# Kernel optimization log

Hardware: AMD Instinct MI355X
Metric: run time of the kernel (lower is better)

The kernel has to match this reference:

```python
import jax, jax.numpy as jnp
import numpy as np

N = 262144          # total nodes in batched graph
B = 2048            # number of graphs
IN_DIM = 512        # in_dim == hidden_dim (required by GRUCell usage)
HID = 512
OUT_DIM = 128
TIMESTEPS = 2


def setup_inputs() -> dict:
    key = jax.random.key(0)
    ks = jax.random.split(key, 12)
    s = 0.02
    x = jax.random.normal(ks[0], (N, IN_DIM), dtype=jnp.float32)
    # sorted random segment ids: ragged graph sizes, node -> graph id
    segment_ids = jnp.sort(jax.random.randint(ks[1], (N,), 0, B, dtype=jnp.int32))
    return {
        "x": x,
        "segment_ids": segment_ids,
        "w_att_l": jax.random.normal(ks[2], (IN_DIM,), dtype=jnp.float32) * s,
        "w_att_r": jax.random.normal(ks[3], (IN_DIM,), dtype=jnp.float32) * s,
        "W_node": jax.random.normal(ks[4], (IN_DIM, HID), dtype=jnp.float32) * s,
        "W_ih": jax.random.normal(ks[5], (3 * HID, HID), dtype=jnp.float32) * s,
        "W_hh": jax.random.normal(ks[6], (3 * HID, HID), dtype=jnp.float32) * s,
        "b_ih": jax.random.normal(ks[7], (3 * HID,), dtype=jnp.float32) * s,
        "b_hh": jax.random.normal(ks[8], (3 * HID,), dtype=jnp.float32) * s,
        "W_lin": jax.random.normal(ks[9], (HID, OUT_DIM), dtype=jnp.float32) * s,
        "b_lin": jax.random.normal(ks[10], (OUT_DIM,), dtype=jnp.float32) * s,
    }


def _segment_softmax(alpha, seg, num_segments):
    # numerically stable per-graph softmax over nodes
    m = jax.ops.segment_max(alpha, seg, num_segments=num_segments)
    e = jnp.exp(alpha - m[seg])
    denom = jax.ops.segment_sum(e, seg, num_segments=num_segments)
    return e / denom[seg]


def _gru_cell(inp, h, W_ih, W_hh, b_ih, b_hh):
    gi = inp @ W_ih.T + b_ih          # [B, 3H]
    gh = h @ W_hh.T + b_hh            # [B, 3H]
    gi_r, gi_z, gi_n = jnp.split(gi, 3, axis=-1)
    gh_r, gh_z, gh_n = jnp.split(gh, 3, axis=-1)
    r = jax.nn.sigmoid(gi_r + gh_r)
    z = jax.nn.sigmoid(gi_z + gh_z)
    n = jnp.tanh(gi_n + r * gh_n)
    return (1.0 - z) * n + z * h


def reference(x, segment_ids, w_att_l, w_att_r, W_node, W_ih, W_hh, b_ih, b_hh, W_lin, b_lin):
    seg = segment_ids
    # SumPooling: per-graph sum of node features -> initial GRU hidden state
    out = jax.ops.segment_sum(x, seg, num_segments=B)      # [B, IN_DIM]
    # src_feats (x) are constant across timesteps -> precompute projections
    left_att = x @ w_att_l                                  # [N]
    h_neighbors = x @ W_node                                # [N, HID]
    for _ in range(TIMESTEPS):
        right_att = out @ w_att_r                           # [B]
        alpha = jax.nn.leaky_relu(left_att + right_att[seg], negative_slope=0.01)
        scores = _segment_softmax(alpha, seg, B)            # [N]
        msg = h_neighbors * scores[:, None]                 # [N, HID]
        gat_out = jax.ops.segment_sum(msg, seg, num_segments=B)  # [B, HID]
        h = jax.nn.elu(gat_out)
        # dropout is identity in eval mode
        out = jax.nn.silu(_gru_cell(h, out, W_ih, W_hh, b_ih, b_hh))
    return out @ W_lin + b_lin                              # [B, OUT_DIM]
```

## Files before the change

### kernel.cpp

```cpp
#include <hip/hip_runtime.h>
#include <hip/hip_bf16.h>
#include <cstdint>
#include <cstddef>

#define N_NODES 262144
#define NGRAPH  2048
#define DIM     512
#define HID3    1536
#define OUTD    128

typedef __attribute__((ext_vector_type(8))) short  short8;
typedef __attribute__((ext_vector_type(4))) float  floatx4;
typedef __attribute__((ext_vector_type(2))) float  floatx2;

__device__ inline unsigned short f2bf(float f) {
    union { float f; uint32_t u; } v; v.f = f;
    uint32_t u = v.u;
    return (unsigned short)((u + 0x7fffu + ((u >> 16) & 1u)) >> 16);
}
__device__ inline float bf2f(unsigned short h) {
    union { uint32_t u; float f; } v; v.u = ((uint32_t)h) << 16; return v.f;
}

__device__ __forceinline__ void gload_lds16(const void* g, void* l) {
    __builtin_amdgcn_global_load_lds((const __attribute__((address_space(1))) void*)g,
                                     (__attribute__((address_space(3))) void*)l, 16, 0, 0);
}

__global__ __launch_bounds__(256) void k_prep(const float* __restrict__ Wih,
        const float* __restrict__ Whh, const float* __restrict__ Wnode,
        const int* __restrict__ seg, unsigned short* __restrict__ Wihb,
        unsigned short* __restrict__ Whhb, unsigned short* __restrict__ WnT,
        int* __restrict__ starts) {
    __shared__ float tile[32][33];
    int id = blockIdx.x, t = threadIdx.x;
    if (id < 3072) {
        int i = id * 256 + t; Wihb[i] = f2bf(Wih[i]);
    } else if (id < 6144) {
        int i = (id - 3072) * 256 + t; Whhb[i] = f2bf(Whh[i]);
    } else if (id < 6400) {
        int idx = id - 6144;
        int bx = idx >> 4, by = idx & 15;
        int tx = t & 31, ty = t >> 5;
        for (int r = 0; r < 32; r += 8)
            tile[ty + r][tx] = Wnode[(size_t)(bx * 32 + ty + r) * DIM + by * 32 + tx];
        __syncthreads();
        for (int r = 0; r < 32; r += 8)
            WnT[(size_t)(by * 32 + ty + r) * DIM + bx * 32 + tx] = f2bf(tile[tx][ty + r]);
    } else {
        int b = (id - 6400) * 256 + t;
        if (b <= NGRAPH) {
            int lo = 0, hi = N_NODES;
            while (lo < hi) { int mid = (lo + hi) >> 1; if (seg[mid] < b) lo = mid + 1; else hi = mid; }
            starts[b] = lo;
        }
    }
}

template<bool WRITE_XQ>
__global__ __launch_bounds__(256) void k_init(const float* __restrict__ x,
        const int* __restrict__ starts, const float* __restrict__ watl,
        float* __restrict__ left_att, float* __restrict__ hcur,
        unsigned short* __restrict__ hcur_bf, unsigned char* __restrict__ xq) {
    __shared__ float wl[DIM];
    __shared__ float red[4 * DIM];
    int b = blockIdx.x, t = threadIdx.x;
    wl[t] = watl[t]; wl[t + 256] = watl[t + 256];
    __syncthreads();
    int s = starts[b], e = starts[b + 1];
    int w = t >> 6, lane = t & 63;
    int f0 = lane * 4;
    float acc[8] = {0.f,0.f,0.f,0.f,0.f,0.f,0.f,0.f};

    auto proc = [&](int i, const float4& v0, const float4& v1) {
        acc[0] += v0.x; acc[1] += v0.y; acc[2] += v0.z; acc[3] += v0.w;
        acc[4] += v1.x; acc[5] += v1.y; acc[6] += v1.z; acc[7] += v1.w;
        float dot = v0.x*wl[f0] + v0.y*wl[f0+1] + v0.z*wl[f0+2] + v0.w*wl[f0+3]
                  + v1.x*wl[256+f0] + v1.y*wl[256+f0+1] + v1.z*wl[256+f0+2] + v1.w*wl[256+f0+3];
        #pragma unroll
        for (int off = 32; off > 0; off >>= 1) dot += __shfl_xor(dot, off);
        if (lane == 0) left_att[i] = dot;
        if constexpr (WRITE_XQ) {
            unsigned int q0 = (unsigned int)__builtin_amdgcn_cvt_pk_fp8_f32(v0.x, v0.y, 0, false);
            q0 = (unsigned int)__builtin_amdgcn_cvt_pk_fp8_f32(v0.z, v0.w, (int)q0, true);
            unsigned int q1 = (unsigned int)__builtin_amdgcn_cvt_pk_fp8_f32(v1.x, v1.y, 0, false);
            q1 = (unsigned int)__builtin_amdgcn_cvt_pk_fp8_f32(v1.z, v1.w, (int)q1, true);
            *reinterpret_cast<unsigned int*>(xq + (size_t)i * DIM + f0) = q0;
            *reinterpret_cast<unsigned int*>(xq + (size_t)i * DIM + 256 + f0) = q1;
        }
    };

    int i = s + w;
    for (; i + 4 < e; i += 8) {
        float4 a0 = *reinterpret_cast<const float4*>(x + (size_t)i * DIM + f0);
        float4 a1 = *reinterpret_cast<const float4*>(x + (size_t)i * DIM + 256 + f0);
        float4 b0 = *reinterpret_cast<const float4*>(x + (size_t)(i + 4) * DIM + f0);
        float4 b1 = *reinterpret_cast<const float4*>(x + (size_t)(i + 4) * DIM + 256 + f0);
        proc(i, a0, a1);
        proc(i + 4, b0, b1);
    }
    if (i < e) {
        float4 a0 = *reinterpret_cast<const float4*>(x + (size_t)i * DIM + f0);
        float4 a1 = *reinterpret_cast<const float4*>(x + (size_t)i * DIM + 256 + f0);
        proc(i, a0, a1);
    }

    #pragma unroll
    for (int j = 0; j < 4; j++) {
        red[w * DIM + f0 + j]       = acc[j];
        red[w * DIM + 256 + f0 + j] = acc[4 + j];
    }
    __syncthreads();
    float s0 = red[t]       + red[DIM + t]       + red[2*DIM + t]       + red[3*DIM + t];
    float s1 = red[256 + t] + red[DIM + 256 + t] + red[2*DIM + 256 + t] + red[3*DIM + 256 + t];
    hcur[(size_t)b * DIM + t] = s0;
    hcur[(size_t)b * DIM + 256 + t] = s1;
    hcur_bf[(size_t)b * DIM + t] = f2bf(s0);
    hcur_bf[(size_t)b * DIM + 256 + t] = f2bf(s1);
}

template<bool XQ>
__global__ __launch_bounds__(256) void k_att(const float* __restrict__ x,
        const unsigned char* __restrict__ xq, const float* __restrict__ left,
        const int* __restrict__ starts, const float* __restrict__ hcur,
        const float* __restrict__ watr, unsigned short* __restrict__ swbf) {
    __shared__ float red[4 * DIM];
    __shared__ float rscal[8];
    int b = blockIdx.x, t = threadIdx.x;
    int w = t >> 6, lane = t & 63;

    float p = hcur[(size_t)b * DIM + t] * watr[t] + hcur[(size_t)b * DIM + 256 + t] * watr[256 + t];
    red[t] = p; __syncthreads();
    for (int off = 128; off > 0; off >>= 1) { if (t < off) red[t] += red[t + off]; __syncthreads(); }
    float ra = red[0];
    __syncthreads();

    int s = starts[b], e = starts[b + 1];
    float m = -1e30f;
    for (int i = s + t; i < e; i += 256) {
        float a = left[i] + ra; a = a >= 0.f ? a : 0.01f * a;
        m = fmaxf(m, a);
    }
    red[t] = m; __syncthreads();
    for (int off = 128; off > 0; off >>= 1) { if (t < off) red[t] = fmaxf(red[t], red[t + off]); __syncthreads(); }
    m = red[0];
    __syncthreads();

    float acc[8] = {0.f,0.f,0.f,0.f,0.f,0.f,0.f,0.f};
    float esum = 0.f;
    if constexpr (XQ) {
        int f0 = lane * 8;
        auto qacc = [&](uint2 q, float ev) {
            floatx2 p0 = __builtin_amdgcn_cvt_pk_f32_fp8((int)q.x, false);
            floatx2 p1 = __builtin_amdgcn_cvt_pk_f32_fp8((int)q.x, true);
            floatx2 p2 = __builtin_amdgcn_cvt_pk_f32_fp8((int)q.y, false);
            floatx2 p3 = __builtin_amdgcn_cvt_pk_f32_fp8((int)q.y, true);
            acc[0] += ev * p0[0]; acc[1] += ev * p0[1];
            acc[2] += ev * p1[0]; acc[3] += ev * p1[1];
            acc[4] += ev * p2[0]; acc[5] += ev * p2[1];
            acc[6] += ev * p3[0]; acc[7] += ev * p3[1];
        };
        int i = s + w;
        for (; i + 4 < e; i += 8) {
            uint2 q0 = *reinterpret_cast<const uint2*>(xq + (size_t)i * DIM + f0);
            uint2 q1 = *reinterpret_cast<const uint2*>(xq + (size_t)(i + 4) * DIM + f0);
            float l0 = left[i], l1 = left[i + 4];
            float a0 = l0 + ra; a0 = a0 >= 0.f ? a0 : 0.01f * a0;
            float a1 = l1 + ra; a1 = a1 >= 0.f ? a1 : 0.01f * a1;
            float e0 = __expf(a0 - m), e1 = __expf(a1 - m);
            esum += e0 + e1;
            qacc(q0, e0);
            qacc(q1, e1);
        }
        if (i < e) {
            uint2 q0 = *reinterpret_cast<const uint2*>(xq + (size_t)i * DIM + f0);
            float a0 = left[i] + ra; a0 = a0 >= 0.f ? a0 : 0.01f * a0;
            float e0 = __expf(a0 - m);
            esum += e0;
            qacc(q0, e0);
        }
        #pragma unroll
        for (int j = 0; j < 8; j++) red[w * DIM + f0 + j] = acc[j];
    } else {
        int f0 = lane * 4;
        for (int i = s + w; i < e; i += 4) {
            float a0 = left[i] + ra; a0 = a0 >= 0.f ? a0 : 0.01f * a0;
            float e0 = __expf(a0 - m);
            esum += e0;
            float4 v0 = *reinterpret_cast<const float4*>(x + (size_t)i * DIM + f0);
            float4 v1 = *reinterpret_cast<const float4*>(x + (size_t)i * DIM + 256 + f0);
            acc[0] += e0 * v0.x; acc[1] += e0 * v0.y; acc[2] += e0 * v0.z; acc[3] += e0 * v0.w;
            acc[4] += e0 * v1.x; acc[5] += e0 * v1.y; acc[6] += e0 * v1.z; acc[7] += e0 * v1.w;
        }
        #pragma unroll
        for (int j = 0; j < 4; j++) {
            red[w * DIM + f0 + j]       = acc[j];
            red[w * DIM + 256 + f0 + j] = acc[4 + j];
        }
    }
    #pragma unroll
    for (int off = 32; off > 0; off >>= 1) esum += __shfl_xor(esum, off);
    if (lane == 0) rscal[w] = esum;
    __syncthreads();
    float tot = rscal[0] + rscal[1] + rscal[2] + rscal[3];
    float inv = tot > 0.f ? 1.0f / tot : 0.0f;
    float s0 = (red[t]       + red[DIM + t]       + red[2*DIM + t]       + red[3*DIM + t])       * inv;
    float s1 = (red[256 + t] + red[DIM + 256 + t] + red[2*DIM + 256 + t] + red[3*DIM + 256 + t]) * inv;
    swbf[(size_t)b * DIM + t] = f2bf(s0);
    swbf[(size_t)b * DIM + 256 + t] = f2bf(s1);
}

template<bool ELU_BF>
__global__ __launch_bounds__(256, 2) void k_gemm(const unsigned short* __restrict__ A0,
        const unsigned short* __restrict__ A1, const unsigned short* __restrict__ Wt0,
        const unsigned short* __restrict__ Wt1, float* __restrict__ Cf0,
        float* __restrict__ Cf1, unsigned short* __restrict__ Cbf, int Ncols) {
    __shared__ __align__(16) unsigned short lA[2][128 * 64];
    __shared__ __align__(16) unsigned short lW[2][128 * 64];
    const unsigned short* A  = (blockIdx.z == 0) ? A0  : A1;
    const unsigned short* Wt = (blockIdx.z == 0) ? Wt0 : Wt1;
    float* Cf = (blockIdx.z == 0) ? Cf0 : Cf1;

    int t = threadIdx.x;
    int w = t >> 6, lane = t & 63;
    int wr = w >> 1, wc = w & 1;
    int mbase = blockIdx.x * 128;
    int nbase = blockIdx.y * 128;
    int fr = lane & 15, hi = lane >> 4;
    int swz_r = (fr & 7) << 4;

    int rbase = t >> 3;
    int cole = ((((t & 7) * 16) ^ ((rbase & 7) << 4)) >> 1);
    int ldsoff = t * 16;

    floatx4 acc[4][4];
    #pragma unroll
    for (int m = 0; m < 4; m++)
        #pragma unroll
        for (int n = 0; n < 4; n++) {
            acc[m][n][0] = 0.f; acc[m][n][1] = 0.f; acc[m][n][2] = 0.f; acc[m][n][3] = 0.f;
        }

    const unsigned short* gA = A  + (size_t)(mbase + rbase) * DIM + cole;
    const unsigned short* gW = Wt + (size_t)(nbase + rbase) * DIM + cole;

    auto stage = [&](int kk, int buf) {
        #pragma unroll
        for (int c = 0; c < 4; ++c) {
            gload_lds16(gA + (size_t)(c * 32) * DIM + kk, (char*)&lA[buf][0] + c * 4096 + ldsoff);
            gload_lds16(gW + (size_t)(c * 32) * DIM + kk, (char*)&lW[buf][0] + c * 4096 + ldsoff);
        }
    };

    stage(0, 0);
    __syncthreads();
    int cur = 0;
    for (int it = 0; it < 8; ++it) {
        if (it < 7) stage((it + 1) * 64, cur ^ 1);
        #pragma unroll
        for (int ks = 0; ks < 2; ++ks) {
            short8 af[4], bf[4];
            int bc = (ks * 64 + hi * 16) ^ swz_r;
            #pragma unroll
            for (int m = 0; m < 4; ++m) {
                int row = wr * 64 + m * 16 + fr;
                af[m] = *reinterpret_cast<const short8*>(&lA[cur][(row * 128 + bc) >> 1]);
            }
            #pragma unroll
            for (int n = 0; n < 4; ++n) {
                int row = wc * 64 + n * 16 + fr;
                bf[n] = *reinterpret_cast<const short8*>(&lW[cur][(row * 128 + bc) >> 1]);
            }
            #pragma unroll
            for (int m = 0; m < 4; ++m)
                #pragma unroll
                for (int n = 0; n < 4; ++n)
                    acc[m][n] = __builtin_amdgcn_mfma_f32_16x16x32_bf16(af[m], bf[n], acc[m][n], 0, 0, 0);
        }
        if (it < 7) __syncthreads();
        cur ^= 1;
    }

    int rq = hi * 4;
    #pragma unroll
    for (int m = 0; m < 4; m++) {
        #pragma unroll
        for (int n = 0; n < 4; n++) {
            int col = nbase + wc * 64 + n * 16 + fr;
            #pragma unroll
            for (int r = 0; r < 4; r++) {
                int row = mbase + wr * 64 + m * 16 + rq + r;
                float v = acc[m][n][r];
                if constexpr (ELU_BF) {
                    v = v > 0.f ? v : (__expf(v) - 1.0f);
                    Cbf[(size_t)row * Ncols + col] = f2bf(v);
                } else {
                    Cf[(size_t)row * Ncols + col] = v;
                }
            }
        }
    }
}

__global__ __launch_bounds__(256) void k_gate(const float* __restrict__ gi,
        const float* __restrict__ gh, const float* __restrict__ bih,
        const float* __restrict__ bhh, float* __restrict__ hcur,
        unsigned short* __restrict__ hcur_bf) {
    int idx = blockIdx.x * 256 + threadIdx.x;
    int b = idx >> 9, j = idx & 511;
    size_t gb = (size_t)b * HID3;
    float gir = gi[gb + j]        + bih[j];
    float giz = gi[gb + 512 + j]  + bih[512 + j];
    float gin = gi[gb + 1024 + j] + bih[1024 + j];
    float ghr = gh[gb + j]        + bhh[j];
    float ghz = gh[gb + 512 + j]  + bhh[512 + j];
    float ghn = gh[gb + 1024 + j] + bhh[1024 + j];
    float r = 1.0f / (1.0f + __expf(-(gir + ghr)));
    float z = 1.0f / (1.0f + __expf(-(giz + ghz)));
    float n = tanhf(gin + r * ghn);
    float h = hcur[(size_t)b * DIM + j];
    float nh = (1.0f - z) * n + z * h;
    float out = nh / (1.0f + __expf(-nh));
    hcur[(size_t)b * DIM + j] = out;
    hcur_bf[(size_t)b * DIM + j] = f2bf(out);
}

__global__ __launch_bounds__(128) void k_fin(const float* __restrict__ hcur,
        const float* __restrict__ Wlin, const float* __restrict__ blin,
        float* __restrict__ out) {
    __shared__ float rows[16 * DIM];
    int t = threadIdx.x;
    int b0 = blockIdx.x * 16;
    for (int i = t; i < 16 * DIM / 4; i += 128)
        reinterpret_cast<float4*>(rows)[i] = reinterpret_cast<const float4*>(hcur + (size_t)b0 * DIM)[i];
    __syncthreads();
    float acc[16];
    #pragma unroll
    for (int r = 0; r < 16; r++) acc[r] = 0.f;
    #pragma unroll 4
    for (int k = 0; k < DIM; k++) {
        float wv = Wlin[k * OUTD + t];
        #pragma unroll
        for (int r = 0; r < 16; r++) acc[r] += rows[r * DIM + k] * wv;
    }
    float bl = blin[t];
    #pragma unroll
    for (int r = 0; r < 16; r++) out[(size_t)(b0 + r) * OUTD + t] = acc[r] + bl;
}

extern "C" void kernel_launch(void* const* d_in, const int* in_sizes, int n_in,
                              void* d_out, int out_size, void* d_ws, size_t ws_size,
                              hipStream_t stream) {
    const float* x     = (const float*)d_in[0];
    const int*   seg   = (const int*)d_in[1];
    const float* watl  = (const float*)d_in[2];
    const float* watr  = (const float*)d_in[3];
    const float* Wnode = (const float*)d_in[4];
    const float* Wih   = (const float*)d_in[5];
    const float* Whh   = (const float*)d_in[6];
    const float* bih   = (const float*)d_in[7];
    const float* bhh   = (const float*)d_in[8];
    const float* Wlin  = (const float*)d_in[9];
    const float* blin  = (const float*)d_in[10];
    float* out = (float*)d_out;

    char* ws = (char*)d_ws;
    size_t off = 0;
    auto alloc = [&](size_t bytes) -> void* {
        void* p = ws + off;
        off += bytes;
        off = (off + 255) & ~(size_t)255;
        return p;
    };
    float*          left    = (float*)          alloc((size_t)N_NODES * sizeof(float));
    float*          hcur    = (float*)          alloc((size_t)NGRAPH * DIM * sizeof(float));
    unsigned short* hcurbf  = (unsigned short*) alloc((size_t)NGRAPH * DIM * 2);
    unsigned short* hgbf    = (unsigned short*) alloc((size_t)NGRAPH * DIM * 2);
    unsigned short* swbf    = (unsigned short*) alloc((size_t)NGRAPH * DIM * 2);
    float*          gi      = (float*)          alloc((size_t)NGRAPH * HID3 * sizeof(float));
    float*          gh      = (float*)          alloc((size_t)NGRAPH * HID3 * sizeof(float));
    unsigned short* WnT     = (unsigned short*) alloc((size_t)DIM * DIM * 2);
    unsigned short* Wihb    = (unsigned short*) alloc((size_t)HID3 * DIM * 2);
    unsigned short* Whhb    = (unsigned short*) alloc((size_t)HID3 * DIM * 2);
    unsigned char*  xq      = (unsigned char*)(ws + off);
    bool use_xq = (off + (size_t)N_NODES * DIM) <= ws_size;

    k_prep<<<6409, 256, 0, stream>>>(Wih, Whh, Wnode, seg, Wihb, Whhb, WnT,
                                     (int*)alloc(0));

    int* starts = (int*)alloc((NGRAPH + 1) * sizeof(int));
    xq = (unsigned char*)(ws + off);
    use_xq = (off + (size_t)N_NODES * DIM) <= ws_size;

    if (use_xq)
        k_init<true ><<<NGRAPH, 256, 0, stream>>>(x, starts, watl, left, hcur, hcurbf, xq);
    else
        k_init<false><<<NGRAPH, 256, 0, stream>>>(x, starts, watl, left, hcur, hcurbf, nullptr);

    for (int ts = 0; ts < 2; ts++) {
        if (use_xq)
            k_att<true ><<<NGRAPH, 256, 0, stream>>>(x, xq, left, starts, hcur, watr, swbf);
        else
            k_att<false><<<NGRAPH, 256, 0, stream>>>(x, xq, left, starts, hcur, watr, swbf);
        k_gemm<true ><<<dim3(NGRAPH / 128, DIM / 128, 1), 256, 0, stream>>>(
            swbf, nullptr, WnT, nullptr, nullptr, nullptr, hgbf, DIM);
        k_gemm<false><<<dim3(NGRAPH / 128, HID3 / 128, 2), 256, 0, stream>>>(
            hgbf, hcurbf, Wihb, Whhb, gi, gh, nullptr, HID3);
        k_gate<<<(NGRAPH * DIM) / 256, 256, 0, stream>>>(gi, gh, bih, bhh, hcur, hcurbf);
    }
    k_fin<<<NGRAPH / 16, 128, 0, stream>>>(hcur, Wlin, blin, out);
}
```

Before: 349.5 us.

## Merge Wnode and Whh GEMMs into one launch, vectorize gate, shuffle reductions

The Wnode projection GEMM and the hidden-state Whh GEMM now share one launch through blockIdx.z, since they are independent, and the Wih GEMM runs afterwards. This gives the node GEMM more concurrent blocks and removes one kernel launch's worth of serialization. The GRU gate kernel now processes four elements per thread with vector loads. The attention kernel's block reductions use wave shuffles instead of shared-memory tree loops, and k_init loads x with nontemporal loads. In exchange, the merged launch has idle z=0 blocks that exit early, and the GEMM takes a runtime branch on whether to write the bf16 output.

```diff
diff --git a/kernel.cpp b/kernel.cpp
--- a/kernel.cpp
+++ b/kernel.cpp
@@ -72,19 +72,19 @@
     int f0 = lane * 4;
     float acc[8] = {0.f,0.f,0.f,0.f,0.f,0.f,0.f,0.f};
 
-    auto proc = [&](int i, const float4& v0, const float4& v1) {
-        acc[0] += v0.x; acc[1] += v0.y; acc[2] += v0.z; acc[3] += v0.w;
-        acc[4] += v1.x; acc[5] += v1.y; acc[6] += v1.z; acc[7] += v1.w;
-        float dot = v0.x*wl[f0] + v0.y*wl[f0+1] + v0.z*wl[f0+2] + v0.w*wl[f0+3]
-                  + v1.x*wl[256+f0] + v1.y*wl[256+f0+1] + v1.z*wl[256+f0+2] + v1.w*wl[256+f0+3];
+    auto proc = [&](int i, floatx4 v0, floatx4 v1) {
+        acc[0] += v0[0]; acc[1] += v0[1]; acc[2] += v0[2]; acc[3] += v0[3];
+        acc[4] += v1[0]; acc[5] += v1[1]; acc[6] += v1[2]; acc[7] += v1[3];
+        float dot = v0[0]*wl[f0] + v0[1]*wl[f0+1] + v0[2]*wl[f0+2] + v0[3]*wl[f0+3]
+                  + v1[0]*wl[256+f0] + v1[1]*wl[256+f0+1] + v1[2]*wl[256+f0+2] + v1[3]*wl[256+f0+3];
         #pragma unroll
         for (int off = 32; off > 0; off >>= 1) dot += __shfl_xor(dot, off);
         if (lane == 0) left_att[i] = dot;
         if constexpr (WRITE_XQ) {
-            unsigned int q0 = (unsigned int)__builtin_amdgcn_cvt_pk_fp8_f32(v0.x, v0.y, 0, false);
-            q0 = (unsigned int)__builtin_amdgcn_cvt_pk_fp8_f32(v0.z, v0.w, (int)q0, true);
-            unsigned int q1 = (unsigned int)__builtin_amdgcn_cvt_pk_fp8_f32(v1.x, v1.y, 0, false);
-            q1 = (unsigned int)__builtin_amdgcn_cvt_pk_fp8_f32(v1.z, v1.w, (int)q1, true);
+            unsigned int q0 = (unsigned int)__builtin_amdgcn_cvt_pk_fp8_f32(v0[0], v0[1], 0, false);
+            q0 = (unsigned int)__builtin_amdgcn_cvt_pk_fp8_f32(v0[2], v0[3], (int)q0, true);
+            unsigned int q1 = (unsigned int)__builtin_amdgcn_cvt_pk_fp8_f32(v1[0], v1[1], 0, false);
+            q1 = (unsigned int)__builtin_amdgcn_cvt_pk_fp8_f32(v1[2], v1[3], (int)q1, true);
             *reinterpret_cast<unsigned int*>(xq + (size_t)i * DIM + f0) = q0;
             *reinterpret_cast<unsigned int*>(xq + (size_t)i * DIM + 256 + f0) = q1;
         }
@@ -92,16 +92,16 @@
 
     int i = s + w;
     for (; i + 4 < e; i += 8) {
-        float4 a0 = *reinterpret_cast<const float4*>(x + (size_t)i * DIM + f0);
-        float4 a1 = *reinterpret_cast<const float4*>(x + (size_t)i * DIM + 256 + f0);
-        float4 b0 = *reinterpret_cast<const float4*>(x + (size_t)(i + 4) * DIM + f0);
-        float4 b1 = *reinterpret_cast<const float4*>(x + (size_t)(i + 4) * DIM + 256 + f0);
+        floatx4 a0 = __builtin_nontemporal_load(reinterpret_cast<const floatx4*>(x + (size_t)i * DIM + f0));
+        floatx4 a1 = __builtin_nontemporal_load(reinterpret_cast<const floatx4*>(x + (size_t)i * DIM + 256 + f0));
+        floatx4 b0 = __builtin_nontemporal_load(reinterpret_cast<const floatx4*>(x + (size_t)(i + 4) * DIM + f0));
+        floatx4 b1 = __builtin_nontemporal_load(reinterpret_cast<const floatx4*>(x + (size_t)(i + 4) * DIM + 256 + f0));
         proc(i, a0, a1);
         proc(i + 4, b0, b1);
     }
     if (i < e) {
-        float4 a0 = *reinterpret_cast<const float4*>(x + (size_t)i * DIM + f0);
-        float4 a1 = *reinterpret_cast<const float4*>(x + (size_t)i * DIM + 256 + f0);
+        floatx4 a0 = __builtin_nontemporal_load(reinterpret_cast<const floatx4*>(x + (size_t)i * DIM + f0));
+        floatx4 a1 = __builtin_nontemporal_load(reinterpret_cast<const floatx4*>(x + (size_t)i * DIM + 256 + f0));
         proc(i, a0, a1);
     }
 
@@ -125,26 +125,30 @@
         const int* __restrict__ starts, const float* __restrict__ hcur,
         const float* __restrict__ watr, unsigned short* __restrict__ swbf) {
     __shared__ float red[4 * DIM];
-    __shared__ float rscal[8];
+    __shared__ float rsh[4];
+    __shared__ float rsm[4];
+    __shared__ float rscal[4];
     int b = blockIdx.x, t = threadIdx.x;
     int w = t >> 6, lane = t & 63;
 
     float p = hcur[(size_t)b * DIM + t] * watr[t] + hcur[(size_t)b * DIM + 256 + t] * watr[256 + t];
-    red[t] = p; __syncthreads();
-    for (int off = 128; off > 0; off >>= 1) { if (t < off) red[t] += red[t + off]; __syncthreads(); }
-    float ra = red[0];
-    __syncthreads();
-
+    #pragma unroll
+    for (int off = 32; off > 0; off >>= 1) p += __shfl_xor(p, off);
+    if (lane == 0) rsh[w] = p;
     int s = starts[b], e = starts[b + 1];
+    __syncthreads();
+    float ra = rsh[0] + rsh[1] + rsh[2] + rsh[3];
+
     float m = -1e30f;
     for (int i = s + t; i < e; i += 256) {
         float a = left[i] + ra; a = a >= 0.f ? a : 0.01f * a;
         m = fmaxf(m, a);
     }
-    red[t] = m; __syncthreads();
-    for (int off = 128; off > 0; off >>= 1) { if (t < off) red[t] = fmaxf(red[t], red[t + off]); __syncthreads(); }
-    m = red[0];
-    __syncthreads();
+    #pragma unroll
+    for (int off = 32; off > 0; off >>= 1) m = fmaxf(m, __shfl_xor(m, off));
+    if (lane == 0) rsm[w] = m;
+    __syncthreads();
+    m = fmaxf(fmaxf(rsm[0], rsm[1]), fmaxf(rsm[2], rsm[3]));
 
     float acc[8] = {0.f,0.f,0.f,0.f,0.f,0.f,0.f,0.f};
     float esum = 0.f;
@@ -164,9 +168,8 @@
         for (; i + 4 < e; i += 8) {
             uint2 q0 = *reinterpret_cast<const uint2*>(xq + (size_t)i * DIM + f0);
             uint2 q1 = *reinterpret_cast<const uint2*>(xq + (size_t)(i + 4) * DIM + f0);
-            float l0 = left[i], l1 = left[i + 4];
-            float a0 = l0 + ra; a0 = a0 >= 0.f ? a0 : 0.01f * a0;
-            float a1 = l1 + ra; a1 = a1 >= 0.f ? a1 : 0.01f * a1;
+            float a0 = left[i] + ra;     a0 = a0 >= 0.f ? a0 : 0.01f * a0;
+            float a1 = left[i + 4] + ra; a1 = a1 >= 0.f ? a1 : 0.01f * a1;
             float e0 = __expf(a0 - m), e1 = __expf(a1 - m);
             esum += e0 + e1;
             qacc(q0, e0);
@@ -210,16 +213,21 @@
     swbf[(size_t)b * DIM + 256 + t] = f2bf(s1);
 }
 
-template<bool ELU_BF>
 __global__ __launch_bounds__(256, 2) void k_gemm(const unsigned short* __restrict__ A0,
-        const unsigned short* __restrict__ A1, const unsigned short* __restrict__ Wt0,
-        const unsigned short* __restrict__ Wt1, float* __restrict__ Cf0,
-        float* __restrict__ Cf1, unsigned short* __restrict__ Cbf, int Ncols) {
+        const unsigned short* __restrict__ Wt0, float* __restrict__ Cf0,
+        unsigned short* __restrict__ Cb0, int Ncols0, int ny0,
+        const unsigned short* __restrict__ A1, const unsigned short* __restrict__ Wt1,
+        float* __restrict__ Cf1, unsigned short* __restrict__ Cb1, int Ncols1) {
+    const int z = blockIdx.z;
+    if (z == 0 && (int)blockIdx.y >= ny0) return;
+    const unsigned short* A  = z ? A1  : A0;
+    const unsigned short* Wt = z ? Wt1 : Wt0;
+    float* Cf          = z ? Cf1 : Cf0;
+    unsigned short* Cb = z ? Cb1 : Cb0;
+    const int Ncols    = z ? Ncols1 : Ncols0;
+
     __shared__ __align__(16) unsigned short lA[2][128 * 64];
     __shared__ __align__(16) unsigned short lW[2][128 * 64];
-    const unsigned short* A  = (blockIdx.z == 0) ? A0  : A1;
-    const unsigned short* Wt = (blockIdx.z == 0) ? Wt0 : Wt1;
-    float* Cf = (blockIdx.z == 0) ? Cf0 : Cf1;
 
     int t = threadIdx.x;
     int w = t >> 6, lane = t & 63;
@@ -291,9 +299,9 @@
             for (int r = 0; r < 4; r++) {
                 int row = mbase + wr * 64 + m * 16 + rq + r;
                 float v = acc[m][n][r];
-                if constexpr (ELU_BF) {
+                if (Cb) {
                     v = v > 0.f ? v : (__expf(v) - 1.0f);
-                    Cbf[(size_t)row * Ncols + col] = f2bf(v);
+                    Cb[(size_t)row * Ncols + col] = f2bf(v);
                 } else {
                     Cf[(size_t)row * Ncols + col] = v;
                 }
@@ -307,22 +315,35 @@
         const float* __restrict__ bhh, float* __restrict__ hcur,
         unsigned short* __restrict__ hcur_bf) {
     int idx = blockIdx.x * 256 + threadIdx.x;
-    int b = idx >> 9, j = idx & 511;
+    int b = idx >> 7, j = (idx & 127) << 2;
     size_t gb = (size_t)b * HID3;
-    float gir = gi[gb + j]        + bih[j];
-    float giz = gi[gb + 512 + j]  + bih[512 + j];
-    float gin = gi[gb + 1024 + j] + bih[1024 + j];
-    float ghr = gh[gb + j]        + bhh[j];
-    float ghz = gh[gb + 512 + j]  + bhh[512 + j];
-    float ghn = gh[gb + 1024 + j] + bhh[1024 + j];
-    float r = 1.0f / (1.0f + __expf(-(gir + ghr)));
-    float z = 1.0f / (1.0f + __expf(-(giz + ghz)));
-    float n = tanhf(gin + r * ghn);
-    float h = hcur[(size_t)b * DIM + j];
-    float nh = (1.0f - z) * n + z * h;
-    float out = nh / (1.0f + __expf(-nh));
-    hcur[(size_t)b * DIM + j] = out;
-    hcur_bf[(size_t)b * DIM + j] = f2bf(out);
+    floatx4 gir = *reinterpret_cast<const floatx4*>(gi + gb + j);
+    floatx4 giz = *reinterpret_cast<const floatx4*>(gi + gb + 512 + j);
+    floatx4 gin = *reinterpret_cast<const floatx4*>(gi + gb + 1024 + j);
+    floatx4 ghr = *reinterpret_cast<const floatx4*>(gh + gb + j);
+    floatx4 ghz = *reinterpret_cast<const floatx4*>(gh + gb + 512 + j);
+    floatx4 ghn = *reinterpret_cast<const floatx4*>(gh + gb + 1024 + j);
+    floatx4 bir = *reinterpret_cast<const floatx4*>(bih + j);
+    floatx4 biz = *reinterpret_cast<const floatx4*>(bih + 512 + j);
+    floatx4 bin = *reinterpret_cast<const floatx4*>(bih + 1024 + j);
+    floatx4 bhr = *reinterpret_cast<const floatx4*>(bhh + j);
+    floatx4 bhz = *reinterpret_cast<const floatx4*>(bhh + 512 + j);
+    floatx4 bhn = *reinterpret_cast<const floatx4*>(bhh + 1024 + j);
+    floatx4 hp  = *reinterpret_cast<const floatx4*>(hcur + (size_t)b * DIM + j);
+    floatx4 ov;
+    ushort4 ob;
+    #pragma unroll
+    for (int r = 0; r < 4; r++) {
+        float rg = 1.0f / (1.0f + __expf(-(gir[r] + bir[r] + ghr[r] + bhr[r])));
+        float zg = 1.0f / (1.0f + __expf(-(giz[r] + biz[r] + ghz[r] + bhz[r])));
+        float nn = tanhf(gin[r] + bin[r] + rg * (ghn[r] + bhn[r]));
+        float nh = (1.0f - zg) * nn + zg * hp[r];
+        float o = nh / (1.0f + __expf(-nh));
+        ov[r] = o;
+        reinterpret_cast<unsigned short*>(&ob)[r] = f2bf(o);
+    }
+    *reinterpret_cast<floatx4*>(hcur + (size_t)b * DIM + j) = ov;
+    *reinterpret_cast<ushort4*>(hcur_bf + (size_t)b * DIM + j) = ob;
 }
 
 __global__ __launch_bounds__(128) void k_fin(const float* __restrict__ hcur,
@@ -382,15 +403,11 @@
     unsigned short* WnT     = (unsigned short*) alloc((size_t)DIM * DIM * 2);
     unsigned short* Wihb    = (unsigned short*) alloc((size_t)HID3 * DIM * 2);
     unsigned short* Whhb    = (unsigned short*) alloc((size_t)HID3 * DIM * 2);
+    int*            starts  = (int*)            alloc((NGRAPH + 1) * sizeof(int));
     unsigned char*  xq      = (unsigned char*)(ws + off);
     bool use_xq = (off + (size_t)N_NODES * DIM) <= ws_size;
 
-    k_prep<<<6409, 256, 0, stream>>>(Wih, Whh, Wnode, seg, Wihb, Whhb, WnT,
-                                     (int*)alloc(0));
-
-    int* starts = (int*)alloc((NGRAPH + 1) * sizeof(int));
-    xq = (unsigned char*)(ws + off);
-    use_xq = (off + (size_t)N_NODES * DIM) <= ws_size;
+    k_prep<<<6409, 256, 0, stream>>>(Wih, Whh, Wnode, seg, Wihb, Whhb, WnT, starts);
 
     if (use_xq)
         k_init<true ><<<NGRAPH, 256, 0, stream>>>(x, starts, watl, left, hcur, hcurbf, xq);
@@ -402,11 +419,13 @@
             k_att<true ><<<NGRAPH, 256, 0, stream>>>(x, xq, left, starts, hcur, watr, swbf);
         else
             k_att<false><<<NGRAPH, 256, 0, stream>>>(x, xq, left, starts, hcur, watr, swbf);
-        k_gemm<true ><<<dim3(NGRAPH / 128, DIM / 128, 1), 256, 0, stream>>>(
-            swbf, nullptr, WnT, nullptr, nullptr, nullptr, hgbf, DIM);
-        k_gemm<false><<<dim3(NGRAPH / 128, HID3 / 128, 2), 256, 0, stream>>>(
-            hgbf, hcurbf, Wihb, Whhb, gi, gh, nullptr, HID3);
-        k_gate<<<(NGRAPH * DIM) / 256, 256, 0, stream>>>(gi, gh, bih, bhh, hcur, hcurbf);
+        k_gemm<<<dim3(NGRAPH / 128, HID3 / 128, 2), 256, 0, stream>>>(
+            swbf, WnT, nullptr, hgbf, DIM, DIM / 128,
+            hcurbf, Whhb, gh, nullptr, HID3);
+        k_gemm<<<dim3(NGRAPH / 128, HID3 / 128, 1), 256, 0, stream>>>(
+            hgbf, Wihb, gi, nullptr, HID3, HID3 / 128,
+            nullptr, nullptr, nullptr, nullptr, 0);
+        k_gate<<<(NGRAPH * 128) / 256, 256, 0, stream>>>(gi, gh, bih, bhh, hcur, hcurbf);
     }
     k_fin<<<NGRAPH / 16, 128, 0, stream>>>(hcur, Wlin, blin, out);
 }
```

Measured after the change: 301.4 us. 13.7% less time.
